# Performance work log

Hardware: AMD Instinct MI355X
Metric: run time of the kernel (lower is better)

Reference implementation:

```python
import jax, jax.numpy as jnp
import numpy as np

H = 256   # input_size
P = 256   # state_size
BATCH, L = 8, 4096
DT_MIN, DT_MAX = 1e-3, 1e-1
LN_EPS = 1e-5


def _hippo_params():
    # HiPPO-N matrix (num_blocks=1), eigendecomposition in numpy (float64 then cast)
    idx = np.arange(P, dtype=np.float64)
    s = np.sqrt(idx + 0.5)
    A = -np.outer(s, s)
    A = np.tril(A) - np.triu(A, 1)
    np.fill_diagonal(A, -0.5)
    ev, V = np.linalg.eig(A)
    order = np.argsort(ev.real)
    ev, V = ev[order], V[:, order]
    return ev, V


def setup_inputs() -> dict:
    key = jax.random.key(0)
    k_u, = jax.random.split(key, 1)
    ev, V = _hippo_params()
    rng = np.random.default_rng(0)
    log_lambda_real = np.log(-np.clip(ev.real, None, -1e-4)).astype(np.float32)
    lambda_imag = ev.imag.astype(np.float32)
    V_inv = np.linalg.inv(V)
    B_init = rng.standard_normal((P, H)) / np.sqrt(P)
    B_tilde = V_inv @ B_init.astype(np.complex128)
    C_init = rng.standard_normal((H, P)) / np.sqrt(P)
    C_tilde = C_init.astype(np.complex128) @ V
    log_delta = (rng.random(P) * (np.log(DT_MAX) - np.log(DT_MIN)) + np.log(DT_MIN)).astype(np.float32)
    return {
        "u": jax.random.normal(k_u, (BATCH, L, H), dtype=jnp.float32),
        "log_lambda_real": jnp.asarray(log_lambda_real),
        "lambda_imag": jnp.asarray(lambda_imag),
        "B_tilde_real": jnp.asarray(B_tilde.real, dtype=jnp.float32),
        "B_tilde_imag": jnp.asarray(B_tilde.imag, dtype=jnp.float32),
        "C_tilde_real": jnp.asarray(C_tilde.real, dtype=jnp.float32),
        "C_tilde_imag": jnp.asarray(C_tilde.imag, dtype=jnp.float32),
        "log_delta": jnp.asarray(log_delta),
        "gamma": jnp.ones((H,), dtype=jnp.float32),
        "beta": jnp.zeros((H,), dtype=jnp.float32),
    }


def _layernorm(x, gamma, beta):
    mu = jnp.mean(x, axis=-1, keepdims=True)
    var = jnp.mean(jnp.square(x - mu), axis=-1, keepdims=True)
    return (x - mu) * jax.lax.rsqrt(var + LN_EPS) * gamma + beta


def _ssm(h, log_lambda_real, lambda_imag, B_tilde_real, B_tilde_imag,
         C_tilde_real, C_tilde_imag, log_delta):
    # Continuous-time diagonal SSM params
    lam = -jnp.exp(log_lambda_real) + 1j * lambda_imag            # (P,) complex
    B_tilde = B_tilde_real + 1j * B_tilde_imag                     # (P,H)
    C_tilde = C_tilde_real + 1j * C_tilde_imag                     # (H,P)
    delta = jnp.exp(log_delta)                                     # (P,)
    # ZOH discretization (eq. 6 of the S5 paper)
    lambda_bar = jnp.exp(lam * delta)                              # (P,)
    B_bar = ((lambda_bar - 1.0) / lam)[:, None] * B_tilde          # (P,H)
    # Bu_k = B_bar @ u_k  ->  (B,L,P) complex
    Bu = jnp.einsum('blh,ph->blp', h.astype(jnp.complex64), B_bar.astype(jnp.complex64))
    # Parallel associative scan for x_k = lambda_bar * x_{k-1} + Bu_k
    a = jnp.broadcast_to(lambda_bar.astype(jnp.complex64), Bu.shape)
    def combine(c1, c2):
        a1, b1 = c1
        a2, b2 = c2
        return a1 * a2, a2 * b1 + b2
    _, xs = jax.lax.associative_scan(combine, (a, Bu), axis=1)     # (B,L,P)
    # Project back to real output: y = Re(C_tilde @ x)
    y = jnp.einsum('blp,hp->blh', xs, C_tilde.astype(jnp.complex64)).real
    return y


def reference(u, log_lambda_real, lambda_imag, B_tilde_real, B_tilde_imag,
              C_tilde_real, C_tilde_imag, log_delta, gamma, beta):
    # S5Block: pre-LayerNorm -> S5 SSM -> GELU -> residual
    h = _layernorm(u, gamma, beta)
    y = _ssm(h, log_lambda_real, lambda_imag, B_tilde_real, B_tilde_imag,
             C_tilde_real, C_tilde_imag, log_delta)
    return u + jax.nn.gelu(y)
```

## Files before the change

kernel.cpp:

```cpp
#include <hip/hip_runtime.h>
#include <math.h>

#define HDIM 256
#define PDIM 256
#define BATCH 8
#define LSEQ 4096
#define MTOT (BATCH * LSEQ)
#define NCHUNK 128
#define CHLEN 32

typedef __attribute__((ext_vector_type(8))) short bf16x8;
typedef __attribute__((ext_vector_type(4))) float f32x4;

__device__ __forceinline__ unsigned short f2bf(float f) {
    union { float f; unsigned int u; } v; v.f = f;
    unsigned int r = v.u + 0x7FFFu + ((v.u >> 16) & 1u);
    return (unsigned short)(r >> 16);
}
__device__ __forceinline__ float bf2f(unsigned int lo16) {
    union { unsigned int u; float f; } v; v.u = lo16 << 16;
    return v.f;
}

__device__ __forceinline__ void gload_lds16(const void* g, void* l) {
    __builtin_amdgcn_global_load_lds(
        (const __attribute__((address_space(1))) void*)g,
        (__attribute__((address_space(3))) void*)l, 16, 0, 0);
}

__global__ void params_k(const float* __restrict__ llr, const float* __restrict__ lim,
                         const float* __restrict__ ldl, float* __restrict__ par) {
    int p = threadIdx.x;
    float er = expf(llr[p]);
    float im = lim[p];
    float d  = expf(ldl[p]);
    float zr = -er * d, zi = im * d;
    float ea = expf(zr);
    float ar = ea * cosf(zi), ai = ea * sinf(zi);
    float dr = -er, di = im;
    float den = dr * dr + di * di;
    float nr = ar - 1.0f, ni = ai;
    float cr = (nr * dr + ni * di) / den;
    float ci = (ni * dr - nr * di) / den;
    float eC = expf((float)CHLEN * zr);
    float sC, cC;
    sincosf((float)CHLEN * zi, &sC, &cC);
    par[2 * p]           = ar;
    par[2 * p + 1]       = ai;
    par[512 + 2 * p]     = cr;
    par[512 + 2 * p + 1] = ci;
    par[1024 + 2 * p]     = eC * cC;
    par[1024 + 2 * p + 1] = eC * sC;
}

__global__ void wpack_k(const float* __restrict__ llr, const float* __restrict__ lim,
                        const float* __restrict__ ldl,
                        const float* __restrict__ Br, const float* __restrict__ Bi,
                        const float* __restrict__ Cr, const float* __restrict__ Ci,
                        unsigned short* __restrict__ W1t, unsigned short* __restrict__ W2t) {
    int h = threadIdx.x;
    if (blockIdx.x < PDIM) {
        int p = blockIdx.x;
        float er = expf(llr[p]);
        float im = lim[p];
        float d  = expf(ldl[p]);
        float zr = -er * d, zi = im * d;
        float ea = expf(zr);
        float sz, cz; sincosf(zi, &sz, &cz);
        float ar = ea * cz, ai = ea * sz;
        float dr = -er, di = im;
        float den = dr * dr + di * di;
        float nr = ar - 1.0f, ni = ai;
        float cr = (nr * dr + ni * di) / den;
        float ci = (ni * dr - nr * di) / den;
        float br = Br[p * HDIM + h], bi = Bi[p * HDIM + h];
        W1t[(2 * p) * HDIM + h]     = f2bf(cr * br - ci * bi);
        W1t[(2 * p + 1) * HDIM + h] = f2bf(cr * bi + ci * br);
    } else {
        int p = blockIdx.x - PDIM;
        W2t[h * (2 * PDIM) + 2 * p]     = f2bf(Cr[h * PDIM + p]);
        W2t[h * (2 * PDIM) + 2 * p + 1] = f2bf(-Ci[h * PDIM + p]);
    }
}

__global__ void ln_k(const float* __restrict__ u, unsigned short* __restrict__ hbf,
                     const float* __restrict__ gamma, const float* __restrict__ beta) {
    __shared__ float gS[HDIM], bS[HDIM];
    int t = threadIdx.x;
    gS[t] = gamma[t]; bS[t] = beta[t];
    int lane = t & 63, wv = t >> 6;
    int row = blockIdx.x * 4 + wv;
    float4 v = *(const float4*)(u + (size_t)row * HDIM + lane * 4);
    float s  = v.x + v.y + v.z + v.w;
    float sq = v.x * v.x + v.y * v.y + v.z * v.z + v.w * v.w;
    #pragma unroll
    for (int o = 1; o < 64; o <<= 1) { s += __shfl_xor(s, o); sq += __shfl_xor(sq, o); }
    float mu = s * (1.0f / HDIM);
    float rs = rsqrtf(sq * (1.0f / HDIM) - mu * mu + 1e-5f);
    __syncthreads();
    int c = lane * 4;
    ushort4 o;
    o.x = f2bf((v.x - mu) * rs * gS[c + 0] + bS[c + 0]);
    o.y = f2bf((v.y - mu) * rs * gS[c + 1] + bS[c + 1]);
    o.z = f2bf((v.z - mu) * rs * gS[c + 2] + bS[c + 2]);
    o.w = f2bf((v.w - mu) * rs * gS[c + 3] + bS[c + 3]);
    *(ushort4*)(hbf + (size_t)row * HDIM + c) = o;
}

template <int MODE, int K>
__launch_bounds__(256, 2)
__global__ void mfma_gemm_k(const unsigned short* __restrict__ A,
                            const unsigned short* __restrict__ B,
                            void* __restrict__ outv,
                            const float* __restrict__ u,
                            int N) {
    __shared__ __align__(16) unsigned short As[128 * 32];
    __shared__ __align__(16) unsigned short Bs[128 * 32];
    const int t = threadIdx.x;

    const int nbn  = (int)gridDim.x;
    const int flat = (int)blockIdx.y * nbn + (int)blockIdx.x;
    const int nwg  = nbn * (int)gridDim.y;
    const int tile = (flat & 7) * (nwg >> 3) + (flat >> 3);
    const int bn = tile % nbn, bm = tile / nbn;

    const int lane = t & 63, w = t >> 6;

    const int srow   = 32 * w + (lane >> 2);
    const int schunk = (lane & 3) ^ ((lane >> 3) & 3);
    const unsigned short* gA = A + (size_t)(bm * 128 + srow) * K + schunk * 8;
    const unsigned short* gB = B + (size_t)(bn * 128 + srow) * K + schunk * 8;
    unsigned short* lA0 = &As[(32 * w) * 32];
    unsigned short* lA1 = &As[(32 * w + 16) * 32];
    unsigned short* lB0 = &Bs[(32 * w) * 32];
    unsigned short* lB1 = &Bs[(32 * w + 16) * 32];

    const int wm = (w & 1) * 64;
    const int wn = (w >> 1) * 64;
    const int mrow = lane & 15;
    const int rsw  = (mrow >> 1) & 3;
    const int cch  = lane >> 4;
    const int fcol = ((cch ^ rsw) * 8);

    f32x4 acc[4][4] = {};

    for (int k0 = 0; k0 < K; k0 += 32) {
        __syncthreads();
        gload_lds16(gA + k0,          lA0);
        gload_lds16(gA + 16 * K + k0, lA1);
        gload_lds16(gB + k0,          lB0);
        gload_lds16(gB + 16 * K + k0, lB1);
        __syncthreads();
        bf16x8 fa[4], fb[4];
        #pragma unroll
        for (int i = 0; i < 4; i++) {
            fa[i] = *(const bf16x8*)&As[(wm + i * 16 + mrow) * 32 + fcol];
            fb[i] = *(const bf16x8*)&Bs[(wn + i * 16 + mrow) * 32 + fcol];
        }
        #pragma unroll
        for (int i = 0; i < 4; i++)
            #pragma unroll
            for (int j = 0; j < 4; j++)
                acc[i][j] = __builtin_amdgcn_mfma_f32_16x16x32_bf16(fa[i], fb[j], acc[i][j], 0, 0, 0);
    }

    const int r0 = (lane >> 4) * 4;
    const int c0 = lane & 15;
    #pragma unroll
    for (int i = 0; i < 4; i++) {
        #pragma unroll
        for (int r = 0; r < 4; r++) {
            const size_t rowoff = (size_t)(bm * 128 + wm + i * 16 + r0 + r) * N;
            #pragma unroll
            for (int j = 0; j < 4; j++) {
                const int col_g = bn * 128 + wn + j * 16 + c0;
                float y = acc[i][j][r];
                if (MODE == 0) {
                    ((unsigned short*)outv)[rowoff + col_g] = f2bf(y);
                } else {
                    float z = 0.7978845608f * fmaf(0.044715f * y * y, y, y);
                    float e = __expf(2.0f * z);
                    float th = 1.0f - 2.0f / (e + 1.0f);
                    float g = 0.5f * y * (1.0f + th);
                    ((float*)outv)[rowoff + col_g] = u[rowoff + col_g] + g;
                }
            }
        }
    }
}

__global__ void scan_reduce_k(const unsigned short* __restrict__ Bu,
                              const float* __restrict__ par, float* __restrict__ last) {
    int p = threadIdx.x, c = blockIdx.x, b = blockIdx.y;
    float ar = par[2 * p], ai = par[2 * p + 1];
    float xr = 0.0f, xi = 0.0f;
    const unsigned int* q = (const unsigned int*)(Bu + ((size_t)b * LSEQ + (size_t)c * CHLEN) * 512) + p;
    #pragma unroll 8
    for (int j = 0; j < CHLEN; j++) {
        unsigned int v = q[j * 256];
        float vr = bf2f(v & 0xFFFFu), vi = bf2f(v >> 16);
        float nr = fmaf(ar, xr, fmaf(-ai, xi, vr));
        float ni = fmaf(ar, xi, fmaf(ai, xr, vi));
        xr = nr; xi = ni;
    }
    *(float2*)(last + ((size_t)b * NCHUNK + c) * 512 + 2 * p) = make_float2(xr, xi);
}

__global__ void scan_carry_k(const float* __restrict__ last, float* __restrict__ prefix,
                             const float* __restrict__ par) {
    int p = threadIdx.x, b = blockIdx.x;
    float Ar = par[1024 + 2 * p], Ai = par[1024 + 2 * p + 1];
    float Pr = 0.0f, Pi = 0.0f;
    const float2* lp = (const float2*)(last + (size_t)b * NCHUNK * 512) + p;
    float2* pp = (float2*)(prefix + (size_t)b * NCHUNK * 512) + p;
    for (int c0 = 0; c0 < NCHUNK; c0 += 16) {
        float2 v[16];
        #pragma unroll
        for (int j = 0; j < 16; j++) v[j] = lp[(size_t)(c0 + j) * 256];
        #pragma unroll
        for (int j = 0; j < 16; j++) {
            pp[(size_t)(c0 + j) * 256] = make_float2(Pr, Pi);
            float nr = fmaf(Ar, Pr, fmaf(-Ai, Pi, v[j].x));
            float ni = fmaf(Ar, Pi, fmaf(Ai, Pr, v[j].y));
            Pr = nr; Pi = ni;
        }
    }
}

__global__ void scan_apply_k(unsigned short* __restrict__ Bu, const float* __restrict__ par,
                             const float* __restrict__ prefix) {
    int p = threadIdx.x, c = blockIdx.x, b = blockIdx.y;
    float ar = par[2 * p], ai = par[2 * p + 1];
    float2 P = *(const float2*)(prefix + ((size_t)b * NCHUNK + c) * 512 + 2 * p);
    float xr = P.x, xi = P.y;
    unsigned int* q = (unsigned int*)(Bu + ((size_t)b * LSEQ + (size_t)c * CHLEN) * 512) + p;
    #pragma unroll 8
    for (int j = 0; j < CHLEN; j++) {
        unsigned int v = q[j * 256];
        float vr = bf2f(v & 0xFFFFu), vi = bf2f(v >> 16);
        float nr = fmaf(ar, xr, fmaf(-ai, xi, vr));
        float ni = fmaf(ar, xi, fmaf(ai, xr, vi));
        xr = nr; xi = ni;
        q[j * 256] = (unsigned int)f2bf(xr) | ((unsigned int)f2bf(xi) << 16);
    }
}

extern "C" void kernel_launch(void* const* d_in, const int* in_sizes, int n_in,
                              void* d_out, int out_size, void* d_ws, size_t ws_size,
                              hipStream_t stream) {
    const float* u   = (const float*)d_in[0];
    const float* llr = (const float*)d_in[1];
    const float* lim = (const float*)d_in[2];
    const float* Br  = (const float*)d_in[3];
    const float* Bi  = (const float*)d_in[4];
    const float* Cr  = (const float*)d_in[5];
    const float* Ci  = (const float*)d_in[6];
    const float* ldl = (const float*)d_in[7];
    const float* gam = (const float*)d_in[8];
    const float* bet = (const float*)d_in[9];
    float* out = (float*)d_out;

    float* ws     = (float*)d_ws;
    float* par    = ws;
    float* last   = ws + 2048;
    float* prefix = last + (size_t)BATCH * NCHUNK * 512;
    unsigned short* W1t = (unsigned short*)(prefix + (size_t)BATCH * NCHUNK * 512);
    unsigned short* W2t = W1t + 512 * HDIM;
    unsigned short* hbf = W2t + HDIM * 512;
    unsigned short* Bu  = hbf + (size_t)MTOT * HDIM;

    ln_k<<<MTOT / 4, 256, 0, stream>>>(u, hbf, gam, bet);
    wpack_k<<<2 * PDIM, HDIM, 0, stream>>>(llr, lim, ldl, Br, Bi, Cr, Ci, W1t, W2t);
    params_k<<<1, PDIM, 0, stream>>>(llr, lim, ldl, par);

    mfma_gemm_k<0, HDIM><<<dim3(512 / 128, MTOT / 128), 256, 0, stream>>>(
        hbf, W1t, (void*)Bu, nullptr, 512);

    scan_reduce_k<<<dim3(NCHUNK, BATCH), PDIM, 0, stream>>>(Bu, par, last);
    scan_carry_k<<<BATCH, PDIM, 0, stream>>>(last, prefix, par);
    scan_apply_k<<<dim3(NCHUNK, BATCH), PDIM, 0, stream>>>(Bu, par, prefix);

    mfma_gemm_k<1, 512><<<dim3(HDIM / 128, MTOT / 128), 256, 0, stream>>>(
        Bu, W2t, (void*)out, u, HDIM);
}
```

Baseline: 165.3 us.

## Double-buffer GEMM LDS tiles, vectorize scan kernels, fold params into wpack

```diff
diff --git a/kernel.cpp b/kernel.cpp
--- a/kernel.cpp
+++ b/kernel.cpp
@@ -28,36 +28,12 @@
         (__attribute__((address_space(3))) void*)l, 16, 0, 0);
 }
 
-__global__ void params_k(const float* __restrict__ llr, const float* __restrict__ lim,
-                         const float* __restrict__ ldl, float* __restrict__ par) {
-    int p = threadIdx.x;
-    float er = expf(llr[p]);
-    float im = lim[p];
-    float d  = expf(ldl[p]);
-    float zr = -er * d, zi = im * d;
-    float ea = expf(zr);
-    float ar = ea * cosf(zi), ai = ea * sinf(zi);
-    float dr = -er, di = im;
-    float den = dr * dr + di * di;
-    float nr = ar - 1.0f, ni = ai;
-    float cr = (nr * dr + ni * di) / den;
-    float ci = (ni * dr - nr * di) / den;
-    float eC = expf((float)CHLEN * zr);
-    float sC, cC;
-    sincosf((float)CHLEN * zi, &sC, &cC);
-    par[2 * p]           = ar;
-    par[2 * p + 1]       = ai;
-    par[512 + 2 * p]     = cr;
-    par[512 + 2 * p + 1] = ci;
-    par[1024 + 2 * p]     = eC * cC;
-    par[1024 + 2 * p + 1] = eC * sC;
-}
-
 __global__ void wpack_k(const float* __restrict__ llr, const float* __restrict__ lim,
                         const float* __restrict__ ldl,
                         const float* __restrict__ Br, const float* __restrict__ Bi,
                         const float* __restrict__ Cr, const float* __restrict__ Ci,
-                        unsigned short* __restrict__ W1t, unsigned short* __restrict__ W2t) {
+                        unsigned short* __restrict__ W1t, unsigned short* __restrict__ W2t,
+                        float* __restrict__ par) {
     int h = threadIdx.x;
     if (blockIdx.x < PDIM) {
         int p = blockIdx.x;
@@ -76,10 +52,33 @@
         float br = Br[p * HDIM + h], bi = Bi[p * HDIM + h];
         W1t[(2 * p) * HDIM + h]     = f2bf(cr * br - ci * bi);
         W1t[(2 * p + 1) * HDIM + h] = f2bf(cr * bi + ci * br);
-    } else {
+    } else if (blockIdx.x < 2 * PDIM) {
         int p = blockIdx.x - PDIM;
         W2t[h * (2 * PDIM) + 2 * p]     = f2bf(Cr[h * PDIM + p]);
         W2t[h * (2 * PDIM) + 2 * p + 1] = f2bf(-Ci[h * PDIM + p]);
+    } else {
+        int p = h;
+        float er = expf(llr[p]);
+        float im = lim[p];
+        float d  = expf(ldl[p]);
+        float zr = -er * d, zi = im * d;
+        float ea = expf(zr);
+        float sz, cz; sincosf(zi, &sz, &cz);
+        float ar = ea * cz, ai = ea * sz;
+        float dr = -er, di = im;
+        float den = dr * dr + di * di;
+        float nr = ar - 1.0f, ni = ai;
+        float cr = (nr * dr + ni * di) / den;
+        float ci = (ni * dr - nr * di) / den;
+        float eC = expf((float)CHLEN * zr);
+        float sC, cC;
+        sincosf((float)CHLEN * zi, &sC, &cC);
+        par[2 * p]            = ar;
+        par[2 * p + 1]        = ai;
+        par[512 + 2 * p]      = cr;
+        par[512 + 2 * p + 1]  = ci;
+        par[1024 + 2 * p]     = eC * cC;
+        par[1024 + 2 * p + 1] = eC * sC;
     }
 }
 
@@ -114,8 +113,8 @@
                             void* __restrict__ outv,
                             const float* __restrict__ u,
                             int N) {
-    __shared__ __align__(16) unsigned short As[128 * 32];
-    __shared__ __align__(16) unsigned short Bs[128 * 32];
+    __shared__ __align__(16) unsigned short As[2][128 * 32];
+    __shared__ __align__(16) unsigned short Bs[2][128 * 32];
     const int t = threadIdx.x;
 
     const int nbn  = (int)gridDim.x;
@@ -130,10 +129,8 @@
     const int schunk = (lane & 3) ^ ((lane >> 3) & 3);
     const unsigned short* gA = A + (size_t)(bm * 128 + srow) * K + schunk * 8;
     const unsigned short* gB = B + (size_t)(bn * 128 + srow) * K + schunk * 8;
-    unsigned short* lA0 = &As[(32 * w) * 32];
-    unsigned short* lA1 = &As[(32 * w + 16) * 32];
-    unsigned short* lB0 = &Bs[(32 * w) * 32];
-    unsigned short* lB1 = &Bs[(32 * w + 16) * 32];
+    const int l0 = (32 * w) * 32;
+    const int l1 = (32 * w + 16) * 32;
 
     const int wm = (w & 1) * 64;
     const int wn = (w >> 1) * 64;
@@ -143,25 +140,36 @@
     const int fcol = ((cch ^ rsw) * 8);
 
     f32x4 acc[4][4] = {};
-
-    for (int k0 = 0; k0 < K; k0 += 32) {
-        __syncthreads();
-        gload_lds16(gA + k0,          lA0);
-        gload_lds16(gA + 16 * K + k0, lA1);
-        gload_lds16(gB + k0,          lB0);
-        gload_lds16(gB + 16 * K + k0, lB1);
-        __syncthreads();
+    constexpr int NT = K / 32;
+
+    gload_lds16(gA,          &As[0][l0]);
+    gload_lds16(gA + 16 * K, &As[0][l1]);
+    gload_lds16(gB,          &Bs[0][l0]);
+    gload_lds16(gB + 16 * K, &Bs[0][l1]);
+    __syncthreads();
+
+    #pragma unroll
+    for (int tt = 0; tt < NT; ++tt) {
+        const int cur = tt & 1;
+        if (tt + 1 < NT) {
+            const int k0 = (tt + 1) * 32;
+            gload_lds16(gA + k0,          &As[cur ^ 1][l0]);
+            gload_lds16(gA + 16 * K + k0, &As[cur ^ 1][l1]);
+            gload_lds16(gB + k0,          &Bs[cur ^ 1][l0]);
+            gload_lds16(gB + 16 * K + k0, &Bs[cur ^ 1][l1]);
+        }
         bf16x8 fa[4], fb[4];
         #pragma unroll
         for (int i = 0; i < 4; i++) {
-            fa[i] = *(const bf16x8*)&As[(wm + i * 16 + mrow) * 32 + fcol];
-            fb[i] = *(const bf16x8*)&Bs[(wn + i * 16 + mrow) * 32 + fcol];
+            fa[i] = *(const bf16x8*)&As[cur][(wm + i * 16 + mrow) * 32 + fcol];
+            fb[i] = *(const bf16x8*)&Bs[cur][(wn + i * 16 + mrow) * 32 + fcol];
         }
         #pragma unroll
         for (int i = 0; i < 4; i++)
             #pragma unroll
             for (int j = 0; j < 4; j++)
                 acc[i][j] = __builtin_amdgcn_mfma_f32_16x16x32_bf16(fa[i], fb[j], acc[i][j], 0, 0, 0);
+        __syncthreads();
     }
 
     const int r0 = (lane >> 4) * 4;
@@ -191,19 +199,31 @@
 
 __global__ void scan_reduce_k(const unsigned short* __restrict__ Bu,
                               const float* __restrict__ par, float* __restrict__ last) {
-    int p = threadIdx.x, c = blockIdx.x, b = blockIdx.y;
-    float ar = par[2 * p], ai = par[2 * p + 1];
-    float xr = 0.0f, xi = 0.0f;
-    const unsigned int* q = (const unsigned int*)(Bu + ((size_t)b * LSEQ + (size_t)c * CHLEN) * 512) + p;
+    int t = threadIdx.x;
+    int lane = t & 63, g = t >> 6;
+    int c = blockIdx.x * 4 + g, b = blockIdx.y;
+    int p0 = lane * 4;
+    float4 a01 = *(const float4*)(par + 2 * p0);
+    float4 a23 = *(const float4*)(par + 2 * p0 + 4);
+    float ar[4] = {a01.x, a01.z, a23.x, a23.z};
+    float ai[4] = {a01.y, a01.w, a23.y, a23.w};
+    float xr[4] = {0.f, 0.f, 0.f, 0.f}, xi[4] = {0.f, 0.f, 0.f, 0.f};
+    const uint4* q = (const uint4*)(Bu + ((size_t)b * LSEQ + (size_t)c * CHLEN) * 512) + lane;
     #pragma unroll 8
     for (int j = 0; j < CHLEN; j++) {
-        unsigned int v = q[j * 256];
-        float vr = bf2f(v & 0xFFFFu), vi = bf2f(v >> 16);
-        float nr = fmaf(ar, xr, fmaf(-ai, xi, vr));
-        float ni = fmaf(ar, xi, fmaf(ai, xr, vi));
-        xr = nr; xi = ni;
-    }
-    *(float2*)(last + ((size_t)b * NCHUNK + c) * 512 + 2 * p) = make_float2(xr, xi);
+        uint4 v = q[(size_t)j * 64];
+        unsigned int vv[4] = {v.x, v.y, v.z, v.w};
+        #pragma unroll
+        for (int k = 0; k < 4; k++) {
+            float vr = bf2f(vv[k] & 0xFFFFu), vi = bf2f(vv[k] >> 16);
+            float nr = fmaf(ar[k], xr[k], fmaf(-ai[k], xi[k], vr));
+            float ni = fmaf(ar[k], xi[k], fmaf(ai[k], xr[k], vi));
+            xr[k] = nr; xi[k] = ni;
+        }
+    }
+    float* lp = last + ((size_t)b * NCHUNK + c) * 512 + 2 * p0;
+    *(float4*)lp       = make_float4(xr[0], xi[0], xr[1], xi[1]);
+    *(float4*)(lp + 4) = make_float4(xr[2], xi[2], xr[3], xi[3]);
 }
 
 __global__ void scan_carry_k(const float* __restrict__ last, float* __restrict__ prefix,
@@ -229,19 +249,34 @@
 
 __global__ void scan_apply_k(unsigned short* __restrict__ Bu, const float* __restrict__ par,
                              const float* __restrict__ prefix) {
-    int p = threadIdx.x, c = blockIdx.x, b = blockIdx.y;
-    float ar = par[2 * p], ai = par[2 * p + 1];
-    float2 P = *(const float2*)(prefix + ((size_t)b * NCHUNK + c) * 512 + 2 * p);
-    float xr = P.x, xi = P.y;
-    unsigned int* q = (unsigned int*)(Bu + ((size_t)b * LSEQ + (size_t)c * CHLEN) * 512) + p;
+    int t = threadIdx.x;
+    int lane = t & 63, g = t >> 6;
+    int c = blockIdx.x * 4 + g, b = blockIdx.y;
+    int p0 = lane * 4;
+    float4 a01 = *(const float4*)(par + 2 * p0);
+    float4 a23 = *(const float4*)(par + 2 * p0 + 4);
+    float ar[4] = {a01.x, a01.z, a23.x, a23.z};
+    float ai[4] = {a01.y, a01.w, a23.y, a23.w};
+    const float* pf = prefix + ((size_t)b * NCHUNK + c) * 512 + 2 * p0;
+    float4 P01 = *(const float4*)pf;
+    float4 P23 = *(const float4*)(pf + 4);
+    float xr[4] = {P01.x, P01.z, P23.x, P23.z};
+    float xi[4] = {P01.y, P01.w, P23.y, P23.w};
+    uint4* q = (uint4*)(Bu + ((size_t)b * LSEQ + (size_t)c * CHLEN) * 512) + lane;
     #pragma unroll 8
     for (int j = 0; j < CHLEN; j++) {
-        unsigned int v = q[j * 256];
-        float vr = bf2f(v & 0xFFFFu), vi = bf2f(v >> 16);
-        float nr = fmaf(ar, xr, fmaf(-ai, xi, vr));
-        float ni = fmaf(ar, xi, fmaf(ai, xr, vi));
-        xr = nr; xi = ni;
-        q[j * 256] = (unsigned int)f2bf(xr) | ((unsigned int)f2bf(xi) << 16);
+        uint4 v = q[(size_t)j * 64];
+        unsigned int vv[4] = {v.x, v.y, v.z, v.w};
+        #pragma unroll
+        for (int k = 0; k < 4; k++) {
+            float vr = bf2f(vv[k] & 0xFFFFu), vi = bf2f(vv[k] >> 16);
+            float nr = fmaf(ar[k], xr[k], fmaf(-ai[k], xi[k], vr));
+            float ni = fmaf(ar[k], xi[k], fmaf(ai[k], xr[k], vi));
+            xr[k] = nr; xi[k] = ni;
+            vv[k] = (unsigned int)f2bf(nr) | ((unsigned int)f2bf(ni) << 16);
+        }
+        uint4 o; o.x = vv[0]; o.y = vv[1]; o.z = vv[2]; o.w = vv[3];
+        q[(size_t)j * 64] = o;
     }
 }
 
@@ -270,15 +305,14 @@
     unsigned short* Bu  = hbf + (size_t)MTOT * HDIM;
 
     ln_k<<<MTOT / 4, 256, 0, stream>>>(u, hbf, gam, bet);
-    wpack_k<<<2 * PDIM, HDIM, 0, stream>>>(llr, lim, ldl, Br, Bi, Cr, Ci, W1t, W2t);
-    params_k<<<1, PDIM, 0, stream>>>(llr, lim, ldl, par);
+    wpack_k<<<2 * PDIM + 1, HDIM, 0, stream>>>(llr, lim, ldl, Br, Bi, Cr, Ci, W1t, W2t, par);
 
     mfma_gemm_k<0, HDIM><<<dim3(512 / 128, MTOT / 128), 256, 0, stream>>>(
         hbf, W1t, (void*)Bu, nullptr, 512);
 
-    scan_reduce_k<<<dim3(NCHUNK, BATCH), PDIM, 0, stream>>>(Bu, par, last);
+    scan_reduce_k<<<dim3(NCHUNK / 4, BATCH), 256, 0, stream>>>(Bu, par, last);
     scan_carry_k<<<BATCH, PDIM, 0, stream>>>(last, prefix, par);
-    scan_apply_k<<<dim3(NCHUNK, BATCH), PDIM, 0, stream>>>(Bu, par, prefix);
+    scan_apply_k<<<dim3(NCHUNK / 4, BATCH), 256, 0, stream>>>(Bu, par, prefix);
 
     mfma_gemm_k<1, 512><<<dim3(HDIM / 128, MTOT / 128), 256, 0, stream>>>(
         Bu, W2t, (void*)out, u, HDIM);
```

New measurement: 168.4 us. Within noise of the previous version (+1.8%).
